# Optimization experiments

Hardware: AMD Instinct MI355X
Metric: run time of the kernel (lower is better)

## Reference

```python
import jax, jax.numpy as jnp
import numpy as np

N = 50000        # nodes
E = 1_600_000    # edges (avg degree 32)
D_IN = 128
HID = 256
D_OUT = 128      # must equal D_IN for the residual add


def setup_inputs() -> dict:
    key = jax.random.key(0)
    k0, k1, k2, k3 = jax.random.split(key, 4)
    x = jax.random.normal(k0, (N, D_IN), dtype=jnp.float32)
    edge_index = jax.random.randint(k1, (2, E), 0, N, dtype=jnp.int32)
    # GCNConv params (lin: Linear without bias in PyG, plus additive bias)
    W1 = jax.random.normal(k2, (D_IN, HID), dtype=jnp.float32) / np.sqrt(D_IN)
    b1 = jnp.zeros((HID,), jnp.float32)
    W2 = jax.random.normal(k3, (HID, D_OUT), dtype=jnp.float32) / np.sqrt(HID)
    b2 = jnp.zeros((D_OUT,), jnp.float32)
    return {"x": x, "edge_index": edge_index, "W1": W1, "b1": b1, "W2": W2, "b2": b2}


def _gcn_conv(x, src, dst, norm, W, b, n):
    # PyG GCNConv: transform, gather source features, scale by sym-norm, scatter-add to dst.
    h = x @ W                        # [n, d_out]
    msg = h[src] * norm[:, None]     # [E+n, d_out] gathered messages
    out = jax.ops.segment_sum(msg, dst, num_segments=n)
    return out + b


def reference(x, edge_index, W1, b1, W2, b2):
    n = x.shape[0]
    # add self loops (GCNConv default add_self_loops=True)
    loops = jnp.arange(n, dtype=edge_index.dtype)
    src = jnp.concatenate([edge_index[0], loops])
    dst = jnp.concatenate([edge_index[1], loops])
    # symmetric normalization D^{-1/2} (A+I) D^{-1/2}
    deg = jax.ops.segment_sum(jnp.ones_like(dst, dtype=x.dtype), dst, num_segments=n)
    dinv = jnp.where(deg > 0, jax.lax.rsqrt(deg), 0.0)
    norm = dinv[src] * dinv[dst]
    skip = x  # nn.Identity skip connection
    h = jax.nn.relu(_gcn_conv(x, src, dst, norm, W1, b1, n))
    out = _gcn_conv(h, src, dst, norm, W2, b2, n)
    # classification_layer treated as identity; original .double() cast kept in fp32
    return out + skip
```

## Files before the change

### kernel.cpp

```cpp
#include <hip/hip_runtime.h>

#define D_IN 128
#define HID 256
#define BKT_SHIFT 8
#define BKT_SIZE 256
#define BKT_CAP 10240
#define CHUNK 4096
#define PAD_SLACK 2048
#define LSTR 264

typedef __attribute__((ext_vector_type(8))) short short8;
typedef __attribute__((ext_vector_type(4))) float floatx4;
typedef __attribute__((ext_vector_type(4))) int intx4;

static __device__ __forceinline__ unsigned short f2b(float f) {
  unsigned u = __float_as_uint(f);
  unsigned r = (u + 0x7fffu + ((u >> 16) & 1u)) >> 16;
  return (unsigned short)r;
}

static __device__ __forceinline__ void unpack8(uint4 v, float* f) {
  f[0] = __uint_as_float(v.x << 16); f[1] = __uint_as_float(v.x & 0xffff0000u);
  f[2] = __uint_as_float(v.y << 16); f[3] = __uint_as_float(v.y & 0xffff0000u);
  f[4] = __uint_as_float(v.z << 16); f[5] = __uint_as_float(v.z & 0xffff0000u);
  f[6] = __uint_as_float(v.w << 16); f[7] = __uint_as_float(v.w & 0xffff0000u);
}

static __device__ __forceinline__ void acc_fma(float* acc, uint4 v, float w) {
  float g[8];
  unpack8(v, g);
#pragma unroll
  for (int d = 0; d < 8; ++d) acc[d] = fmaf(g[d], w, acc[d]);
}


__global__ __launch_bounds__(256) void fused_front_kernel(
    const int* __restrict__ src, const int* __restrict__ dst,
    int* __restrict__ bkt_cursor, int* __restrict__ ebuf, int E, int nbkt, int nchunk,
    const float4* __restrict__ x4, unsigned short* __restrict__ xb, int n4,
    const float* __restrict__ W1, unsigned short* __restrict__ Wt1,
    const float* __restrict__ W2, unsigned short* __restrict__ Wt2,
    float* __restrict__ dinv, unsigned short* __restrict__ aggx,
    unsigned short* __restrict__ tb, int N) {
  const int bid = blockIdx.x;
  const int tid = threadIdx.x;
  if (bid < nchunk) {
    __shared__ int hist[BKT_SIZE];
    __shared__ int bbase[BKT_SIZE];
    if (tid < nbkt) hist[tid] = 0;
    __syncthreads();
    const int base = bid * CHUNK;
    const int end = min(base + CHUNK, E);
    for (int e = base + tid; e < end; e += 256)
      atomicAdd(&hist[dst[e] >> BKT_SHIFT], 1);
    __syncthreads();
    if (tid < nbkt) {
      int c = hist[tid];
      bbase[tid] = c > 0 ? atomicAdd(&bkt_cursor[tid], c) : 0;
      hist[tid] = 0;
    }
    __syncthreads();
    for (int e = base + tid; e < end; e += 256) {
      int d = dst[e];
      int b = d >> BKT_SHIFT;
      int off = atomicAdd(&hist[b], 1);
      int rel = bbase[b] + off;
      if (rel < BKT_CAP)
        ebuf[b * BKT_CAP + rel] = (src[e] << BKT_SHIFT) | (d & (BKT_SIZE - 1));
    }
    return;
  }
  const int nxblk = (n4 + 255) / 256;
  if (bid < nchunk + nxblk) {
    int i = (bid - nchunk) * 256 + tid;
    if (i >= n4) return;
    float4 v = x4[i];
    ushort4 o;
    o.x = f2b(v.x); o.y = f2b(v.y); o.z = f2b(v.z); o.w = f2b(v.w);
    *(ushort4*)(xb + (size_t)i * 4) = o;
  } else if (bid < nchunk + nxblk + 128) {
    int e = (bid - nchunk - nxblk) * 256 + tid;
    int k = e >> 8, n = e & 255;
    Wt1[(size_t)n * D_IN + k] = f2b(W1[e]);
  } else if (bid < nchunk + nxblk + 256) {
    int e = (bid - nchunk - nxblk - 128) * 256 + tid;
    int k = e >> 7, n = e & 127;
    Wt2[(size_t)n * HID + k] = f2b(W2[e]);
  } else {
    if (tid == 0) dinv[N] = 0.f;
    if (tid < 64)       ((unsigned*)(xb   + (size_t)N * D_IN))[tid]       = 0u;
    else if (tid < 128) ((unsigned*)(aggx + (size_t)N * D_IN))[tid - 64]  = 0u;
    else if (tid < 192) ((unsigned*)(tb   + (size_t)N * D_IN))[tid - 128] = 0u;
  }
}


__global__ __launch_bounds__(256) void bucket_build_kernel(const int* __restrict__ ebuf,
                                                           const int* __restrict__ bkt_cursor,
                                                           float* __restrict__ dinv,
                                                           int2* __restrict__ rowse,
                                                           int* __restrict__ csr,
                                                           int N, int nbkt) {
  __shared__ int hist[BKT_SIZE];
  __shared__ int srs[BKT_SIZE];
  __shared__ int wsums[4];
  const int b = blockIdx.x;
  const int tid = threadIdx.x;
  const int node0 = b << BKT_SHIFT;
  const int nloc = min(BKT_SIZE, N - node0);
  const int ebeg = b * BKT_CAP;
  const int eend = ebeg + min(bkt_cursor[b], BKT_CAP);

  hist[tid] = 0;
  __syncthreads();
  for (int e = ebeg + tid; e < eend; e += 256)
    atomicAdd(&hist[ebuf[e] & (BKT_SIZE - 1)], 1);
  __syncthreads();

  const int h = hist[tid];
  const int p = (h + 7) & ~7;
  const int lane = tid & 63, wid = tid >> 6;
  int incl = p;
#pragma unroll
  for (int off = 1; off < 64; off <<= 1) {
    int t = __shfl_up(incl, off);
    if (lane >= off) incl += t;
  }
  if (lane == 63) wsums[wid] = incl;
  __syncthreads();
  int wex = 0;
  for (int w = 0; w < wid; ++w) wex += wsums[w];
  const int ex = wex + incl - p;
  const int base = b * (BKT_CAP + PAD_SLACK);
  if (tid < nloc) {
    int st = base + ex;
    dinv[node0 + tid] = rsqrtf((float)(h + 1));
    rowse[node0 + tid] = make_int2(st, st + p);
    srs[tid] = st;
  }
  hist[tid] = 0;
  __syncthreads();

  for (int e = ebeg + tid; e < eend; e += 256) {
    int u = ebuf[e];
    int l = u & (BKT_SIZE - 1);
    int pos = atomicAdd(&hist[l], 1);
    csr[srs[l] + pos] = u >> BKT_SHIFT;
  }
  __syncthreads();
  for (int l = tid; l < nloc; l += 256) {
    int deg = hist[l];
    int pp = (deg + 7) & ~7;
    int s0 = srs[l];
    for (int q = s0 + deg; q < s0 + pp; ++q) csr[q] = N;
  }
}


__global__ __launch_bounds__(256) void gemm12_kernel(const unsigned short* __restrict__ A,
                                                     const unsigned short* __restrict__ Wt1,
                                                     const float* __restrict__ b1,
                                                     const unsigned short* __restrict__ Wt2,
                                                     unsigned short* __restrict__ T, int M) {
  __shared__ unsigned short hs[64][LSTR];
  const int tid = threadIdx.x;
  const int wave = tid >> 6;
  const int lane = tid & 63;
  const int quad = lane >> 4;
  const int l16 = lane & 15;
  const int row0 = blockIdx.x * 64;

  const short8* ap[4];
#pragma unroll
  for (int g = 0; g < 4; ++g) {
    int r = row0 + g * 16 + l16;
    if (r >= M) r = M - 1;
    ap[g] = (const short8*)(A + (size_t)r * D_IN + quad * 8);
  }
  const short8* bp1 = (const short8*)(Wt1 + (size_t)(wave * 64 + l16) * D_IN + quad * 8);

  floatx4 acc1[4][4];
#pragma unroll
  for (int g = 0; g < 4; ++g)
#pragma unroll
    for (int t = 0; t < 4; ++t) acc1[g][t] = floatx4{0.f, 0.f, 0.f, 0.f};

#pragma unroll
  for (int kt = 0; kt < 4; ++kt) {
    short8 a0 = ap[0][kt * 4], a1 = ap[1][kt * 4], a2 = ap[2][kt * 4], a3 = ap[3][kt * 4];
#pragma unroll
    for (int t = 0; t < 4; ++t) {
      short8 b = bp1[kt * 4 + t * 256];
      acc1[0][t] = __builtin_amdgcn_mfma_f32_16x16x32_bf16(a0, b, acc1[0][t], 0, 0, 0);
      acc1[1][t] = __builtin_amdgcn_mfma_f32_16x16x32_bf16(a1, b, acc1[1][t], 0, 0, 0);
      acc1[2][t] = __builtin_amdgcn_mfma_f32_16x16x32_bf16(a2, b, acc1[2][t], 0, 0, 0);
      acc1[3][t] = __builtin_amdgcn_mfma_f32_16x16x32_bf16(a3, b, acc1[3][t], 0, 0, 0);
    }
  }
#pragma unroll
  for (int t = 0; t < 4; ++t) {
    const float bv = b1[wave * 64 + t * 16 + l16];
#pragma unroll
    for (int g = 0; g < 4; ++g)
#pragma unroll
      for (int r = 0; r < 4; ++r) {
        float v = acc1[g][t][r] + bv;
        v = v > 0.f ? v : 0.f;
        hs[g * 16 + quad * 4 + r][wave * 64 + t * 16 + l16] = f2b(v);
      }
  }
  __syncthreads();

  const short8* bp2 = (const short8*)(Wt2 + (size_t)(wave * 32 + l16) * HID + quad * 8);
  floatx4 acc2[4][2];
#pragma unroll
  for (int g = 0; g < 4; ++g)
#pragma unroll
    for (int t = 0; t < 2; ++t) acc2[g][t] = floatx4{0.f, 0.f, 0.f, 0.f};

#pragma unroll
  for (int kt = 0; kt < 8; ++kt) {
    short8 a0 = *(const short8*)&hs[0 * 16 + l16][kt * 32 + quad * 8];
    short8 a1 = *(const short8*)&hs[1 * 16 + l16][kt * 32 + quad * 8];
    short8 a2 = *(const short8*)&hs[2 * 16 + l16][kt * 32 + quad * 8];
    short8 a3 = *(const short8*)&hs[3 * 16 + l16][kt * 32 + quad * 8];
#pragma unroll
    for (int t = 0; t < 2; ++t) {
      short8 b = bp2[kt * 4 + t * 512];
      acc2[0][t] = __builtin_amdgcn_mfma_f32_16x16x32_bf16(a0, b, acc2[0][t], 0, 0, 0);
      acc2[1][t] = __builtin_amdgcn_mfma_f32_16x16x32_bf16(a1, b, acc2[1][t], 0, 0, 0);
      acc2[2][t] = __builtin_amdgcn_mfma_f32_16x16x32_bf16(a2, b, acc2[2][t], 0, 0, 0);
      acc2[3][t] = __builtin_amdgcn_mfma_f32_16x16x32_bf16(a3, b, acc2[3][t], 0, 0, 0);
    }
  }
  __syncthreads();

#pragma unroll
  for (int t = 0; t < 2; ++t)
#pragma unroll
    for (int g = 0; g < 4; ++g)
#pragma unroll
      for (int r = 0; r < 4; ++r)
        hs[g * 16 + quad * 4 + r][wave * 32 + t * 16 + l16] = f2b(acc2[g][t][r]);
  __syncthreads();

#pragma unroll
  for (int i = 0; i < 4; ++i) {
    const int r = i * 16 + (tid >> 4);
    const int c = (tid & 15) * 8;
    const int row = row0 + r;
    uint4 v = *(const uint4*)&hs[r][c];
    if (row < M) *(uint4*)&T[(size_t)row * D_IN + c] = v;
  }
}


template<bool SKIP_BIAS>
__global__ __launch_bounds__(256) void agg_kernel(const uint4* __restrict__ Hq,
                                                  const int2* __restrict__ rowse,
                                                  const int* __restrict__ csr,
                                                  const float* __restrict__ dinv,
                                                  const float* __restrict__ skip,
                                                  const float* __restrict__ bias,
                                                  void* __restrict__ OUT, int n) {
  const int lane = threadIdx.x & 15;
  const int node = blockIdx.x * 16 + (threadIdx.x >> 4);
  if (node >= n) return;

  const float dv = dinv[node];
  float acc[8];
  {
    uint4 sv = Hq[(size_t)node * 16 + lane];
    float f[8];
    unpack8(sv, f);
    const float ws = dv * dv;
#pragma unroll
    for (int d = 0; d < 8; ++d) acc[d] = f[d] * ws;
  }

  const int2 se = rowse[node];
  intx4 c0 = *(const intx4*)(csr + se.x);
  intx4 c1 = *(const intx4*)(csr + se.x + 4);
  for (int j = se.x; j < se.y; ) {
    const int jn = j + 8;
    const int jp = (jn < se.y) ? jn : se.x;
    intx4 n0 = *(const intx4*)(csr + jp);
    intx4 n1 = *(const intx4*)(csr + jp + 4);
    float w0 = dinv[c0.x] * dv, w1 = dinv[c0.y] * dv;
    float w2 = dinv[c0.z] * dv, w3 = dinv[c0.w] * dv;
    float w4 = dinv[c1.x] * dv, w5 = dinv[c1.y] * dv;
    float w6 = dinv[c1.z] * dv, w7 = dinv[c1.w] * dv;
    uint4 v0 = Hq[(size_t)c0.x * 16 + lane];
    uint4 v1 = Hq[(size_t)c0.y * 16 + lane];
    uint4 v2 = Hq[(size_t)c0.z * 16 + lane];
    uint4 v3 = Hq[(size_t)c0.w * 16 + lane];
    uint4 v4 = Hq[(size_t)c1.x * 16 + lane];
    uint4 v5 = Hq[(size_t)c1.y * 16 + lane];
    uint4 v6 = Hq[(size_t)c1.z * 16 + lane];
    uint4 v7 = Hq[(size_t)c1.w * 16 + lane];
    acc_fma(acc, v0, w0);
    acc_fma(acc, v1, w1);
    acc_fma(acc, v2, w2);
    acc_fma(acc, v3, w3);
    acc_fma(acc, v4, w4);
    acc_fma(acc, v5, w5);
    acc_fma(acc, v6, w6);
    acc_fma(acc, v7, w7);
    c0 = n0; c1 = n1; j = jn;
  }

  if (SKIP_BIAS) {
    const float* sp = skip + (size_t)node * 128 + lane * 8;
    const float* bp = bias + lane * 8;
    float4 s0 = *(const float4*)sp, s1 = *(const float4*)(sp + 4);
    float4 b0 = *(const float4*)bp, b1 = *(const float4*)(bp + 4);
    float* op = (float*)OUT + (size_t)node * 128 + lane * 8;
    *(float4*)op = make_float4(acc[0] + s0.x + b0.x, acc[1] + s0.y + b0.y,
                               acc[2] + s0.z + b0.z, acc[3] + s0.w + b0.w);
    *(float4*)(op + 4) = make_float4(acc[4] + s1.x + b1.x, acc[5] + s1.y + b1.y,
                                     acc[6] + s1.z + b1.z, acc[7] + s1.w + b1.w);
  } else {
    uint4 o;
    o.x = (unsigned)f2b(acc[0]) | ((unsigned)f2b(acc[1]) << 16);
    o.y = (unsigned)f2b(acc[2]) | ((unsigned)f2b(acc[3]) << 16);
    o.z = (unsigned)f2b(acc[4]) | ((unsigned)f2b(acc[5]) << 16);
    o.w = (unsigned)f2b(acc[6]) | ((unsigned)f2b(acc[7]) << 16);
    ((uint4*)OUT)[(size_t)node * 16 + lane] = o;
  }
}


extern "C" void kernel_launch(void* const* d_in, const int* in_sizes, int n_in,
                              void* d_out, int out_size, void* d_ws, size_t ws_size,
                              hipStream_t stream) {
  const float* x  = (const float*)d_in[0];
  const int*   ei = (const int*)d_in[1];
  const float* W1 = (const float*)d_in[2];
  const float* b1 = (const float*)d_in[3];
  const float* W2 = (const float*)d_in[4];
  const float* b2 = (const float*)d_in[5];
  float* out = (float*)d_out;

  const int N = in_sizes[0] / D_IN;
  const int E = in_sizes[1] / 2;
  const int* srcA = ei;
  const int* dstA = ei + E;
  const int NBKT = (N + BKT_SIZE - 1) >> BKT_SHIFT;
  const int NCHUNK = (E + CHUNK - 1) / CHUNK;

  char* ws = (char*)d_ws;
  size_t off = 0;
  auto alloc = [&](size_t bytes) { void* p = ws + off; off = (off + bytes + 255) & ~(size_t)255; return p; };
  int*            bkt_cursor = (int*)           alloc((size_t)NBKT * 4);
  float*          dinv       = (float*)         alloc((size_t)(N + 1) * 4);
  int2*           rowse      = (int2*)          alloc((size_t)N * 8);
  int*            ebuf       = (int*)           alloc((size_t)NBKT * BKT_CAP * 4);
  int*            csr        = (int*)           alloc((size_t)NBKT * (BKT_CAP + PAD_SLACK) * 4);
  unsigned short* xb         = (unsigned short*)alloc((size_t)(N + 1) * D_IN * 2);
  unsigned short* aggx       = (unsigned short*)alloc((size_t)(N + 1) * D_IN * 2);
  unsigned short* tb         = (unsigned short*)alloc((size_t)(N + 1) * D_IN * 2);
  unsigned short* Wt1        = (unsigned short*)alloc((size_t)D_IN * HID * 2);
  unsigned short* Wt2        = (unsigned short*)alloc((size_t)D_IN * HID * 2);

  const int n4 = N * D_IN / 4;
  const int nxblk = (n4 + 255) / 256;

  (void)hipMemsetAsync(bkt_cursor, 0, (size_t)NBKT * 4, stream);
  fused_front_kernel<<<NCHUNK + nxblk + 256 + 1, 256, 0, stream>>>(
      srcA, dstA, bkt_cursor, ebuf, E, NBKT, NCHUNK,
      (const float4*)x, xb, n4, W1, Wt1, W2, Wt2, dinv, aggx, tb, N);
  bucket_build_kernel<<<NBKT, 256, 0, stream>>>(ebuf, bkt_cursor, dinv, rowse, csr, N, NBKT);
  agg_kernel<false><<<(N + 15) / 16, 256, 0, stream>>>((const uint4*)xb, rowse, csr,
                                                       dinv, nullptr, nullptr, aggx, N);
  gemm12_kernel<<<(N + 63) / 64, 256, 0, stream>>>(aggx, Wt1, b1, Wt2, tb, N);
  agg_kernel<true><<<(N + 15) / 16, 256, 0, stream>>>((const uint4*)tb, rowse, csr,
                                                      dinv, x, b2, out, N);
}
```

Measured before the change: 272.4 us.

## Fuse first-layer aggregation into the two-layer GEMM kernel via shared memory

The first sparse aggregation now writes its bf16 rows into a shared-memory tile, and the same block runs the W1 and W2 MFMA GEMMs on that tile. This removes the aggx intermediate buffer, one global write and read of it, and one kernel launch. The GEMM tile shrinks from 64 to 32 rows per block, so the weights are reloaded more often and the MFMA work per block is smaller. The gather-bound phase and the GEMM phase now share one block's occupancy and LDS budget.

```diff
diff --git a/kernel.cpp b/kernel.cpp
--- a/kernel.cpp
+++ b/kernel.cpp
@@ -8,6 +8,7 @@
 #define CHUNK 4096
 #define PAD_SLACK 2048
 #define LSTR 264
+#define ASTR 136
 
 typedef __attribute__((ext_vector_type(8))) short short8;
 typedef __attribute__((ext_vector_type(4))) float floatx4;
@@ -33,252 +34,10 @@
   for (int d = 0; d < 8; ++d) acc[d] = fmaf(g[d], w, acc[d]);
 }
 
-
-__global__ __launch_bounds__(256) void fused_front_kernel(
-    const int* __restrict__ src, const int* __restrict__ dst,
-    int* __restrict__ bkt_cursor, int* __restrict__ ebuf, int E, int nbkt, int nchunk,
-    const float4* __restrict__ x4, unsigned short* __restrict__ xb, int n4,
-    const float* __restrict__ W1, unsigned short* __restrict__ Wt1,
-    const float* __restrict__ W2, unsigned short* __restrict__ Wt2,
-    float* __restrict__ dinv, unsigned short* __restrict__ aggx,
-    unsigned short* __restrict__ tb, int N) {
-  const int bid = blockIdx.x;
-  const int tid = threadIdx.x;
-  if (bid < nchunk) {
-    __shared__ int hist[BKT_SIZE];
-    __shared__ int bbase[BKT_SIZE];
-    if (tid < nbkt) hist[tid] = 0;
-    __syncthreads();
-    const int base = bid * CHUNK;
-    const int end = min(base + CHUNK, E);
-    for (int e = base + tid; e < end; e += 256)
-      atomicAdd(&hist[dst[e] >> BKT_SHIFT], 1);
-    __syncthreads();
-    if (tid < nbkt) {
-      int c = hist[tid];
-      bbase[tid] = c > 0 ? atomicAdd(&bkt_cursor[tid], c) : 0;
-      hist[tid] = 0;
-    }
-    __syncthreads();
-    for (int e = base + tid; e < end; e += 256) {
-      int d = dst[e];
-      int b = d >> BKT_SHIFT;
-      int off = atomicAdd(&hist[b], 1);
-      int rel = bbase[b] + off;
-      if (rel < BKT_CAP)
-        ebuf[b * BKT_CAP + rel] = (src[e] << BKT_SHIFT) | (d & (BKT_SIZE - 1));
-    }
-    return;
-  }
-  const int nxblk = (n4 + 255) / 256;
-  if (bid < nchunk + nxblk) {
-    int i = (bid - nchunk) * 256 + tid;
-    if (i >= n4) return;
-    float4 v = x4[i];
-    ushort4 o;
-    o.x = f2b(v.x); o.y = f2b(v.y); o.z = f2b(v.z); o.w = f2b(v.w);
-    *(ushort4*)(xb + (size_t)i * 4) = o;
-  } else if (bid < nchunk + nxblk + 128) {
-    int e = (bid - nchunk - nxblk) * 256 + tid;
-    int k = e >> 8, n = e & 255;
-    Wt1[(size_t)n * D_IN + k] = f2b(W1[e]);
-  } else if (bid < nchunk + nxblk + 256) {
-    int e = (bid - nchunk - nxblk - 128) * 256 + tid;
-    int k = e >> 7, n = e & 127;
-    Wt2[(size_t)n * HID + k] = f2b(W2[e]);
-  } else {
-    if (tid == 0) dinv[N] = 0.f;
-    if (tid < 64)       ((unsigned*)(xb   + (size_t)N * D_IN))[tid]       = 0u;
-    else if (tid < 128) ((unsigned*)(aggx + (size_t)N * D_IN))[tid - 64]  = 0u;
-    else if (tid < 192) ((unsigned*)(tb   + (size_t)N * D_IN))[tid - 128] = 0u;
-  }
-}
-
-
-__global__ __launch_bounds__(256) void bucket_build_kernel(const int* __restrict__ ebuf,
-                                                           const int* __restrict__ bkt_cursor,
-                                                           float* __restrict__ dinv,
-                                                           int2* __restrict__ rowse,
-                                                           int* __restrict__ csr,
-                                                           int N, int nbkt) {
-  __shared__ int hist[BKT_SIZE];
-  __shared__ int srs[BKT_SIZE];
-  __shared__ int wsums[4];
-  const int b = blockIdx.x;
-  const int tid = threadIdx.x;
-  const int node0 = b << BKT_SHIFT;
-  const int nloc = min(BKT_SIZE, N - node0);
-  const int ebeg = b * BKT_CAP;
-  const int eend = ebeg + min(bkt_cursor[b], BKT_CAP);
-
-  hist[tid] = 0;
-  __syncthreads();
-  for (int e = ebeg + tid; e < eend; e += 256)
-    atomicAdd(&hist[ebuf[e] & (BKT_SIZE - 1)], 1);
-  __syncthreads();
-
-  const int h = hist[tid];
-  const int p = (h + 7) & ~7;
-  const int lane = tid & 63, wid = tid >> 6;
-  int incl = p;
-#pragma unroll
-  for (int off = 1; off < 64; off <<= 1) {
-    int t = __shfl_up(incl, off);
-    if (lane >= off) incl += t;
-  }
-  if (lane == 63) wsums[wid] = incl;
-  __syncthreads();
-  int wex = 0;
-  for (int w = 0; w < wid; ++w) wex += wsums[w];
-  const int ex = wex + incl - p;
-  const int base = b * (BKT_CAP + PAD_SLACK);
-  if (tid < nloc) {
-    int st = base + ex;
-    dinv[node0 + tid] = rsqrtf((float)(h + 1));
-    rowse[node0 + tid] = make_int2(st, st + p);
-    srs[tid] = st;
-  }
-  hist[tid] = 0;
-  __syncthreads();
-
-  for (int e = ebeg + tid; e < eend; e += 256) {
-    int u = ebuf[e];
-    int l = u & (BKT_SIZE - 1);
-    int pos = atomicAdd(&hist[l], 1);
-    csr[srs[l] + pos] = u >> BKT_SHIFT;
-  }
-  __syncthreads();
-  for (int l = tid; l < nloc; l += 256) {
-    int deg = hist[l];
-    int pp = (deg + 7) & ~7;
-    int s0 = srs[l];
-    for (int q = s0 + deg; q < s0 + pp; ++q) csr[q] = N;
-  }
-}
-
-
-__global__ __launch_bounds__(256) void gemm12_kernel(const unsigned short* __restrict__ A,
-                                                     const unsigned short* __restrict__ Wt1,
-                                                     const float* __restrict__ b1,
-                                                     const unsigned short* __restrict__ Wt2,
-                                                     unsigned short* __restrict__ T, int M) {
-  __shared__ unsigned short hs[64][LSTR];
-  const int tid = threadIdx.x;
-  const int wave = tid >> 6;
-  const int lane = tid & 63;
-  const int quad = lane >> 4;
-  const int l16 = lane & 15;
-  const int row0 = blockIdx.x * 64;
-
-  const short8* ap[4];
-#pragma unroll
-  for (int g = 0; g < 4; ++g) {
-    int r = row0 + g * 16 + l16;
-    if (r >= M) r = M - 1;
-    ap[g] = (const short8*)(A + (size_t)r * D_IN + quad * 8);
-  }
-  const short8* bp1 = (const short8*)(Wt1 + (size_t)(wave * 64 + l16) * D_IN + quad * 8);
-
-  floatx4 acc1[4][4];
-#pragma unroll
-  for (int g = 0; g < 4; ++g)
-#pragma unroll
-    for (int t = 0; t < 4; ++t) acc1[g][t] = floatx4{0.f, 0.f, 0.f, 0.f};
-
-#pragma unroll
-  for (int kt = 0; kt < 4; ++kt) {
-    short8 a0 = ap[0][kt * 4], a1 = ap[1][kt * 4], a2 = ap[2][kt * 4], a3 = ap[3][kt * 4];
-#pragma unroll
-    for (int t = 0; t < 4; ++t) {
-      short8 b = bp1[kt * 4 + t * 256];
-      acc1[0][t] = __builtin_amdgcn_mfma_f32_16x16x32_bf16(a0, b, acc1[0][t], 0, 0, 0);
-      acc1[1][t] = __builtin_amdgcn_mfma_f32_16x16x32_bf16(a1, b, acc1[1][t], 0, 0, 0);
-      acc1[2][t] = __builtin_amdgcn_mfma_f32_16x16x32_bf16(a2, b, acc1[2][t], 0, 0, 0);
-      acc1[3][t] = __builtin_amdgcn_mfma_f32_16x16x32_bf16(a3, b, acc1[3][t], 0, 0, 0);
-    }
-  }
-#pragma unroll
-  for (int t = 0; t < 4; ++t) {
-    const float bv = b1[wave * 64 + t * 16 + l16];
-#pragma unroll
-    for (int g = 0; g < 4; ++g)
-#pragma unroll
-      for (int r = 0; r < 4; ++r) {
-        float v = acc1[g][t][r] + bv;
-        v = v > 0.f ? v : 0.f;
-        hs[g * 16 + quad * 4 + r][wave * 64 + t * 16 + l16] = f2b(v);
-      }
-  }
-  __syncthreads();
-
-  const short8* bp2 = (const short8*)(Wt2 + (size_t)(wave * 32 + l16) * HID + quad * 8);
-  floatx4 acc2[4][2];
-#pragma unroll
-  for (int g = 0; g < 4; ++g)
-#pragma unroll
-    for (int t = 0; t < 2; ++t) acc2[g][t] = floatx4{0.f, 0.f, 0.f, 0.f};
-
-#pragma unroll
-  for (int kt = 0; kt < 8; ++kt) {
-    short8 a0 = *(const short8*)&hs[0 * 16 + l16][kt * 32 + quad * 8];
-    short8 a1 = *(const short8*)&hs[1 * 16 + l16][kt * 32 + quad * 8];
-    short8 a2 = *(const short8*)&hs[2 * 16 + l16][kt * 32 + quad * 8];
-    short8 a3 = *(const short8*)&hs[3 * 16 + l16][kt * 32 + quad * 8];
-#pragma unroll
-    for (int t = 0; t < 2; ++t) {
-      short8 b = bp2[kt * 4 + t * 512];
-      acc2[0][t] = __builtin_amdgcn_mfma_f32_16x16x32_bf16(a0, b, acc2[0][t], 0, 0, 0);
-      acc2[1][t] = __builtin_amdgcn_mfma_f32_16x16x32_bf16(a1, b, acc2[1][t], 0, 0, 0);
-      acc2[2][t] = __builtin_amdgcn_mfma_f32_16x16x32_bf16(a2, b, acc2[2][t], 0, 0, 0);
-      acc2[3][t] = __builtin_amdgcn_mfma_f32_16x16x32_bf16(a3, b, acc2[3][t], 0, 0, 0);
-    }
-  }
-  __syncthreads();
-
-#pragma unroll
-  for (int t = 0; t < 2; ++t)
-#pragma unroll
-    for (int g = 0; g < 4; ++g)
-#pragma unroll
-      for (int r = 0; r < 4; ++r)
-        hs[g * 16 + quad * 4 + r][wave * 32 + t * 16 + l16] = f2b(acc2[g][t][r]);
-  __syncthreads();
-
-#pragma unroll
-  for (int i = 0; i < 4; ++i) {
-    const int r = i * 16 + (tid >> 4);
-    const int c = (tid & 15) * 8;
-    const int row = row0 + r;
-    uint4 v = *(const uint4*)&hs[r][c];
-    if (row < M) *(uint4*)&T[(size_t)row * D_IN + c] = v;
-  }
-}
-
-
-template<bool SKIP_BIAS>
-__global__ __launch_bounds__(256) void agg_kernel(const uint4* __restrict__ Hq,
-                                                  const int2* __restrict__ rowse,
+static __device__ __forceinline__ void gather_row(float* acc, const uint4* __restrict__ Hq,
+                                                  const float* __restrict__ dinv,
                                                   const int* __restrict__ csr,
-                                                  const float* __restrict__ dinv,
-                                                  const float* __restrict__ skip,
-                                                  const float* __restrict__ bias,
-                                                  void* __restrict__ OUT, int n) {
-  const int lane = threadIdx.x & 15;
-  const int node = blockIdx.x * 16 + (threadIdx.x >> 4);
-  if (node >= n) return;
-
-  const float dv = dinv[node];
-  float acc[8];
-  {
-    uint4 sv = Hq[(size_t)node * 16 + lane];
-    float f[8];
-    unpack8(sv, f);
-    const float ws = dv * dv;
-#pragma unroll
-    for (int d = 0; d < 8; ++d) acc[d] = f[d] * ws;
-  }
-
-  const int2 se = rowse[node];
+                                                  int2 se, float dv, int lane) {
   intx4 c0 = *(const intx4*)(csr + se.x);
   intx4 c1 = *(const intx4*)(csr + se.x + 4);
   for (int j = se.x; j < se.y; ) {
@@ -308,25 +67,276 @@
     acc_fma(acc, v7, w7);
     c0 = n0; c1 = n1; j = jn;
   }
-
-  if (SKIP_BIAS) {
-    const float* sp = skip + (size_t)node * 128 + lane * 8;
-    const float* bp = bias + lane * 8;
-    float4 s0 = *(const float4*)sp, s1 = *(const float4*)(sp + 4);
-    float4 b0 = *(const float4*)bp, b1 = *(const float4*)(bp + 4);
-    float* op = (float*)OUT + (size_t)node * 128 + lane * 8;
-    *(float4*)op = make_float4(acc[0] + s0.x + b0.x, acc[1] + s0.y + b0.y,
-                               acc[2] + s0.z + b0.z, acc[3] + s0.w + b0.w);
-    *(float4*)(op + 4) = make_float4(acc[4] + s1.x + b1.x, acc[5] + s1.y + b1.y,
-                                     acc[6] + s1.z + b1.z, acc[7] + s1.w + b1.w);
+}
+
+
+__global__ __launch_bounds__(256) void fused_front_kernel(
+    const int* __restrict__ src, const int* __restrict__ dst,
+    int* __restrict__ bkt_cursor, int* __restrict__ ebuf, int E, int nbkt, int nchunk,
+    const float4* __restrict__ x4, unsigned short* __restrict__ xb, int n4,
+    const float* __restrict__ W1, unsigned short* __restrict__ Wt1,
+    const float* __restrict__ W2, unsigned short* __restrict__ Wt2,
+    float* __restrict__ dinv, unsigned short* __restrict__ tb, int N) {
+  const int bid = blockIdx.x;
+  const int tid = threadIdx.x;
+  if (bid < nchunk) {
+    __shared__ int hist[BKT_SIZE];
+    __shared__ int bbase[BKT_SIZE];
+    if (tid < nbkt) hist[tid] = 0;
+    __syncthreads();
+    const int base = bid * CHUNK;
+    const int end = min(base + CHUNK, E);
+    for (int e = base + tid; e < end; e += 256)
+      atomicAdd(&hist[dst[e] >> BKT_SHIFT], 1);
+    __syncthreads();
+    if (tid < nbkt) {
+      int c = hist[tid];
+      bbase[tid] = c > 0 ? atomicAdd(&bkt_cursor[tid], c) : 0;
+      hist[tid] = 0;
+    }
+    __syncthreads();
+    for (int e = base + tid; e < end; e += 256) {
+      int d = dst[e];
+      int b = d >> BKT_SHIFT;
+      int off = atomicAdd(&hist[b], 1);
+      int rel = bbase[b] + off;
+      if (rel < BKT_CAP)
+        ebuf[b * BKT_CAP + rel] = (src[e] << BKT_SHIFT) | (d & (BKT_SIZE - 1));
+    }
+    return;
+  }
+  const int nxblk = (n4 + 255) / 256;
+  if (bid < nchunk + nxblk) {
+    int i = (bid - nchunk) * 256 + tid;
+    if (i >= n4) return;
+    float4 v = x4[i];
+    ushort4 o;
+    o.x = f2b(v.x); o.y = f2b(v.y); o.z = f2b(v.z); o.w = f2b(v.w);
+    *(ushort4*)(xb + (size_t)i * 4) = o;
+  } else if (bid < nchunk + nxblk + 128) {
+    int e = (bid - nchunk - nxblk) * 256 + tid;
+    int k = e >> 8, n = e & 255;
+    Wt1[(size_t)n * D_IN + k] = f2b(W1[e]);
+  } else if (bid < nchunk + nxblk + 256) {
+    int e = (bid - nchunk - nxblk - 128) * 256 + tid;
+    int k = e >> 7, n = e & 127;
+    Wt2[(size_t)n * HID + k] = f2b(W2[e]);
   } else {
-    uint4 o;
-    o.x = (unsigned)f2b(acc[0]) | ((unsigned)f2b(acc[1]) << 16);
-    o.y = (unsigned)f2b(acc[2]) | ((unsigned)f2b(acc[3]) << 16);
-    o.z = (unsigned)f2b(acc[4]) | ((unsigned)f2b(acc[5]) << 16);
-    o.w = (unsigned)f2b(acc[6]) | ((unsigned)f2b(acc[7]) << 16);
-    ((uint4*)OUT)[(size_t)node * 16 + lane] = o;
-  }
+    if (tid == 0) dinv[N] = 0.f;
+    if (tid < 64)       ((unsigned*)(xb + (size_t)N * D_IN))[tid]      = 0u;
+    else if (tid < 128) ((unsigned*)(tb + (size_t)N * D_IN))[tid - 64] = 0u;
+  }
+}
+
+
+__global__ __launch_bounds__(256) void bucket_build_kernel(const int* __restrict__ ebuf,
+                                                           const int* __restrict__ bkt_cursor,
+                                                           float* __restrict__ dinv,
+                                                           int2* __restrict__ rowse,
+                                                           int* __restrict__ csr,
+                                                           int N, int nbkt) {
+  __shared__ int hist[BKT_SIZE];
+  __shared__ int srs[BKT_SIZE];
+  __shared__ int wsums[4];
+  const int b = blockIdx.x;
+  const int tid = threadIdx.x;
+  const int node0 = b << BKT_SHIFT;
+  const int nloc = min(BKT_SIZE, N - node0);
+  const int ebeg = b * BKT_CAP;
+  const int eend = ebeg + min(bkt_cursor[b], BKT_CAP);
+
+  hist[tid] = 0;
+  __syncthreads();
+  for (int e = ebeg + tid; e < eend; e += 256)
+    atomicAdd(&hist[ebuf[e] & (BKT_SIZE - 1)], 1);
+  __syncthreads();
+
+  const int h = hist[tid];
+  const int p = (h + 7) & ~7;
+  const int lane = tid & 63, wid = tid >> 6;
+  int incl = p;
+#pragma unroll
+  for (int off = 1; off < 64; off <<= 1) {
+    int t = __shfl_up(incl, off);
+    if (lane >= off) incl += t;
+  }
+  if (lane == 63) wsums[wid] = incl;
+  __syncthreads();
+  int wex = 0;
+  for (int w = 0; w < wid; ++w) wex += wsums[w];
+  const int ex = wex + incl - p;
+  const int base = b * (BKT_CAP + PAD_SLACK);
+  if (tid < nloc) {
+    int st = base + ex;
+    dinv[node0 + tid] = rsqrtf((float)(h + 1));
+    rowse[node0 + tid] = make_int2(st, st + p);
+    srs[tid] = st;
+  }
+  hist[tid] = 0;
+  __syncthreads();
+
+  for (int e = ebeg + tid; e < eend; e += 256) {
+    int u = ebuf[e];
+    int l = u & (BKT_SIZE - 1);
+    int pos = atomicAdd(&hist[l], 1);
+    csr[srs[l] + pos] = u >> BKT_SHIFT;
+  }
+  __syncthreads();
+  for (int l = tid; l < nloc; l += 256) {
+    int deg = hist[l];
+    int pp = (deg + 7) & ~7;
+    int s0 = srs[l];
+    for (int q = s0 + deg; q < s0 + pp; ++q) csr[q] = N;
+  }
+}
+
+
+__global__ __launch_bounds__(256) void agg1_gemm_kernel(
+    const uint4* __restrict__ Hq, const int2* __restrict__ rowse,
+    const int* __restrict__ csr, const float* __restrict__ dinv,
+    const unsigned short* __restrict__ Wt1, const float* __restrict__ b1,
+    const unsigned short* __restrict__ Wt2, unsigned short* __restrict__ T, int M) {
+  __shared__ unsigned short as_[32][ASTR];
+  __shared__ unsigned short hs[32][LSTR];
+  const int tid = threadIdx.x;
+  const int node0 = blockIdx.x * 32;
+
+  {
+    const int glane = tid & 15;
+#pragma unroll
+    for (int g = 0; g < 2; ++g) {
+      const int lrow = g * 16 + (tid >> 4);
+      const int node = node0 + lrow;
+      float acc[8] = {0.f, 0.f, 0.f, 0.f, 0.f, 0.f, 0.f, 0.f};
+      if (node < M) {
+        const float dv = dinv[node];
+        uint4 sv = Hq[(size_t)node * 16 + glane];
+        float f[8];
+        unpack8(sv, f);
+        const float ws = dv * dv;
+#pragma unroll
+        for (int d = 0; d < 8; ++d) acc[d] = f[d] * ws;
+        gather_row(acc, Hq, dinv, csr, rowse[node], dv, glane);
+      }
+      uint4 o;
+      o.x = (unsigned)f2b(acc[0]) | ((unsigned)f2b(acc[1]) << 16);
+      o.y = (unsigned)f2b(acc[2]) | ((unsigned)f2b(acc[3]) << 16);
+      o.z = (unsigned)f2b(acc[4]) | ((unsigned)f2b(acc[5]) << 16);
+      o.w = (unsigned)f2b(acc[6]) | ((unsigned)f2b(acc[7]) << 16);
+      *(uint4*)&as_[lrow][glane * 8] = o;
+    }
+  }
+  __syncthreads();
+
+  const int wave = tid >> 6;
+  const int lane = tid & 63;
+  const int quad = lane >> 4;
+  const int l16 = lane & 15;
+
+  const short8* bp1 = (const short8*)(Wt1 + (size_t)(wave * 64 + l16) * D_IN + quad * 8);
+  floatx4 acc1[2][4];
+#pragma unroll
+  for (int g = 0; g < 2; ++g)
+#pragma unroll
+    for (int t = 0; t < 4; ++t) acc1[g][t] = floatx4{0.f, 0.f, 0.f, 0.f};
+
+#pragma unroll
+  for (int kt = 0; kt < 4; ++kt) {
+    short8 a0 = *(const short8*)&as_[0 * 16 + l16][kt * 32 + quad * 8];
+    short8 a1 = *(const short8*)&as_[1 * 16 + l16][kt * 32 + quad * 8];
+#pragma unroll
+    for (int t = 0; t < 4; ++t) {
+      short8 b = bp1[kt * 4 + t * 256];
+      acc1[0][t] = __builtin_amdgcn_mfma_f32_16x16x32_bf16(a0, b, acc1[0][t], 0, 0, 0);
+      acc1[1][t] = __builtin_amdgcn_mfma_f32_16x16x32_bf16(a1, b, acc1[1][t], 0, 0, 0);
+    }
+  }
+#pragma unroll
+  for (int t = 0; t < 4; ++t) {
+    const float bv = b1[wave * 64 + t * 16 + l16];
+#pragma unroll
+    for (int g = 0; g < 2; ++g)
+#pragma unroll
+      for (int r = 0; r < 4; ++r) {
+        float v = acc1[g][t][r] + bv;
+        v = v > 0.f ? v : 0.f;
+        hs[g * 16 + quad * 4 + r][wave * 64 + t * 16 + l16] = f2b(v);
+      }
+  }
+  __syncthreads();
+
+  const short8* bp2 = (const short8*)(Wt2 + (size_t)(wave * 32 + l16) * HID + quad * 8);
+  floatx4 acc2[2][2];
+#pragma unroll
+  for (int g = 0; g < 2; ++g)
+#pragma unroll
+    for (int t = 0; t < 2; ++t) acc2[g][t] = floatx4{0.f, 0.f, 0.f, 0.f};
+
+#pragma unroll
+  for (int kt = 0; kt < 8; ++kt) {
+    short8 a0 = *(const short8*)&hs[0 * 16 + l16][kt * 32 + quad * 8];
+    short8 a1 = *(const short8*)&hs[1 * 16 + l16][kt * 32 + quad * 8];
+#pragma unroll
+    for (int t = 0; t < 2; ++t) {
+      short8 b = bp2[kt * 4 + t * 512];
+      acc2[0][t] = __builtin_amdgcn_mfma_f32_16x16x32_bf16(a0, b, acc2[0][t], 0, 0, 0);
+      acc2[1][t] = __builtin_amdgcn_mfma_f32_16x16x32_bf16(a1, b, acc2[1][t], 0, 0, 0);
+    }
+  }
+  __syncthreads();
+
+#pragma unroll
+  for (int t = 0; t < 2; ++t)
+#pragma unroll
+    for (int g = 0; g < 2; ++g)
+#pragma unroll
+      for (int r = 0; r < 4; ++r)
+        hs[g * 16 + quad * 4 + r][wave * 32 + t * 16 + l16] = f2b(acc2[g][t][r]);
+  __syncthreads();
+
+#pragma unroll
+  for (int i = 0; i < 2; ++i) {
+    const int r = i * 16 + (tid >> 4);
+    const int c = (tid & 15) * 8;
+    const int row = node0 + r;
+    uint4 v = *(const uint4*)&hs[r][c];
+    if (row < M) *(uint4*)&T[(size_t)row * D_IN + c] = v;
+  }
+}
+
+
+__global__ __launch_bounds__(256) void agg2_kernel(const uint4* __restrict__ Hq,
+                                                   const int2* __restrict__ rowse,
+                                                   const int* __restrict__ csr,
+                                                   const float* __restrict__ dinv,
+                                                   const float* __restrict__ skip,
+                                                   const float* __restrict__ bias,
+                                                   float* __restrict__ OUT, int n) {
+  const int lane = threadIdx.x & 15;
+  const int node = blockIdx.x * 16 + (threadIdx.x >> 4);
+  if (node >= n) return;
+
+  const float dv = dinv[node];
+  float acc[8];
+  {
+    uint4 sv = Hq[(size_t)node * 16 + lane];
+    float f[8];
+    unpack8(sv, f);
+    const float ws = dv * dv;
+#pragma unroll
+    for (int d = 0; d < 8; ++d) acc[d] = f[d] * ws;
+  }
+  gather_row(acc, Hq, dinv, csr, rowse[node], dv, lane);
+
+  const float* sp = skip + (size_t)node * 128 + lane * 8;
+  const float* bp = bias + lane * 8;
+  float4 s0 = *(const float4*)sp, s1 = *(const float4*)(sp + 4);
+  float4 b0 = *(const float4*)bp, b1 = *(const float4*)(bp + 4);
+  float* op = OUT + (size_t)node * 128 + lane * 8;
+  *(float4*)op = make_float4(acc[0] + s0.x + b0.x, acc[1] + s0.y + b0.y,
+                             acc[2] + s0.z + b0.z, acc[3] + s0.w + b0.w);
+  *(float4*)(op + 4) = make_float4(acc[4] + s1.x + b1.x, acc[5] + s1.y + b1.y,
+                                   acc[6] + s1.z + b1.z, acc[7] + s1.w + b1.w);
 }
 
 
@@ -357,7 +367,6 @@
   int*            ebuf       = (int*)           alloc((size_t)NBKT * BKT_CAP * 4);
   int*            csr        = (int*)           alloc((size_t)NBKT * (BKT_CAP + PAD_SLACK) * 4);
   unsigned short* xb         = (unsigned short*)alloc((size_t)(N + 1) * D_IN * 2);
-  unsigned short* aggx       = (unsigned short*)alloc((size_t)(N + 1) * D_IN * 2);
   unsigned short* tb         = (unsigned short*)alloc((size_t)(N + 1) * D_IN * 2);
   unsigned short* Wt1        = (unsigned short*)alloc((size_t)D_IN * HID * 2);
   unsigned short* Wt2        = (unsigned short*)alloc((size_t)D_IN * HID * 2);
@@ -368,11 +377,10 @@
   (void)hipMemsetAsync(bkt_cursor, 0, (size_t)NBKT * 4, stream);
   fused_front_kernel<<<NCHUNK + nxblk + 256 + 1, 256, 0, stream>>>(
       srcA, dstA, bkt_cursor, ebuf, E, NBKT, NCHUNK,
-      (const float4*)x, xb, n4, W1, Wt1, W2, Wt2, dinv, aggx, tb, N);
+      (const float4*)x, xb, n4, W1, Wt1, W2, Wt2, dinv, tb, N);
   bucket_build_kernel<<<NBKT, 256, 0, stream>>>(ebuf, bkt_cursor, dinv, rowse, csr, N, NBKT);
-  agg_kernel<false><<<(N + 15) / 16, 256, 0, stream>>>((const uint4*)xb, rowse, csr,
-                                                       dinv, nullptr, nullptr, aggx, N);
-  gemm12_kernel<<<(N + 63) / 64, 256, 0, stream>>>(aggx, Wt1, b1, Wt2, tb, N);
-  agg_kernel<true><<<(N + 15) / 16, 256, 0, stream>>>((const uint4*)tb, rowse, csr,
-                                                      dinv, x, b2, out, N);
-}
+  agg1_gemm_kernel<<<(N + 31) / 32, 256, 0, stream>>>((const uint4*)xb, rowse, csr, dinv,
+                                                      Wt1, b1, Wt2, tb, N);
+  agg2_kernel<<<(N + 15) / 16, 256, 0, stream>>>((const uint4*)tb, rowse, csr,
+                                                 dinv, x, b2, out, N);
+}
```

Result: faster. 266.7 us (-2.1%).
